# Kernel tuning notes

Measured on AMD Instinct MI355X. Metric: run time of the kernel, lower is better.

Reference implementation:

```python
import jax, jax.numpy as jnp
import numpy as np

N = 50000
E = 1600000
EP = 500000
D_IN, D_EMB = 64, 32


def setup_inputs() -> dict:
    key = jax.random.key(0)
    ks = jax.random.split(key, 12)
    return {
        "x": jax.random.normal(ks[0], (N, D_IN), dtype=jnp.float32),
        "W1": jax.random.normal(ks[1], (D_IN, D_EMB), dtype=jnp.float32) * (1.0 / np.sqrt(D_IN)),
        "b1": jnp.zeros((D_EMB,), dtype=jnp.float32),
        "W2": jax.random.normal(ks[2], (D_EMB, 2 * D_EMB), dtype=jnp.float32) * (1.0 / np.sqrt(D_EMB)),
        "b2": jnp.zeros((2 * D_EMB,), dtype=jnp.float32),
        "eps": jax.random.normal(ks[3], (N, D_EMB), dtype=jnp.float32),
        "edge_src": jax.random.randint(ks[4], (E,), 0, N, dtype=jnp.int32),
        "edge_dst": jax.random.randint(ks[5], (E,), 0, N, dtype=jnp.int32),
        "pos_src": jax.random.randint(ks[6], (EP,), 0, N, dtype=jnp.int32),
        "pos_dst": jax.random.randint(ks[7], (EP,), 0, N, dtype=jnp.int32),
        "neg_src": jax.random.randint(ks[8], (EP,), 0, N, dtype=jnp.int32),
        "neg_dst": jax.random.randint(ks[9], (EP,), 0, N, dtype=jnp.int32),
    }


def _degree_norms(src, dst, n):
    ones = jnp.ones(src.shape, dtype=jnp.float32)
    out_deg = jax.ops.segment_sum(ones, src, num_segments=n)
    in_deg = jax.ops.segment_sum(ones, dst, num_segments=n)
    # DGL GraphConv norm='both': clamp degrees to >=1, pow(-0.5)
    return jnp.clip(out_deg, 1.0) ** -0.5, jnp.clip(in_deg, 1.0) ** -0.5


def _graph_conv(h, src, dst, norm_src, norm_dst, W, b, n):
    # rst = D_dst^{-1/2} A D_src^{-1/2} h W + b
    msg = (h * norm_src[:, None])[src]                       # [E, d] gather
    agg = jax.ops.segment_sum(msg, dst, num_segments=n)      # [N, d] scatter-add
    return (agg * norm_dst[:, None]) @ W + b


def _dot_predict(z, u, v):
    # u_dot_v: per-edge inner product of endpoint embeddings
    return jnp.sum(z[u] * z[v], axis=-1)


def reference(x, W1, b1, W2, b2, eps, edge_src, edge_dst,
              pos_src, pos_dst, neg_src, neg_dst):
    n = x.shape[0]
    ns, nd = _degree_norms(edge_src, edge_dst, n)
    h = _graph_conv(x, edge_src, edge_dst, ns, nd, W1, b1, n)
    h = jax.nn.relu(h)  # dropout = identity (eval mode)
    h = _graph_conv(h, edge_src, edge_dst, ns, nd, W2, b2, n)
    mu, log_var = jnp.split(h, 2, axis=-1)
    sigma = jnp.exp(log_var / 2.0)
    z = mu + sigma * eps
    pos = _dot_predict(z, pos_src, pos_dst)
    neg = _dot_predict(z, neg_src, neg_dst)
    return pos, neg, mu, sigma
```

## Files before the change

### kernel.cpp

```cpp
#include <hip/hip_runtime.h>
#include <math.h>

#define NN  50000
#define NE  1600000
#define NEP 500000
#define DIN 64
#define DE  32

#define BKT_SH 7
#define NB     391
#define S1B    250
#define CHK    6400
#define HB     128
#define HCHK   12500
#define HWRD   12500
#define XWB    3125

__device__ __forceinline__ unsigned f2b(float f) {
    unsigned u = __float_as_uint(f);
    return (u + 0x7FFFu + ((u >> 16) & 1u)) >> 16;
}
__device__ __forceinline__ unsigned pack2(float a, float b) {
    return f2b(a) | (f2b(b) << 16);
}
__device__ __forceinline__ float blo(unsigned u) { return __uint_as_float(u << 16); }
__device__ __forceinline__ float bhi(unsigned u) { return __uint_as_float(u & 0xFFFF0000u); }

__global__ __launch_bounds__(256) void k_h1s1(const int* __restrict__ src,
                                              const int* __restrict__ dst,
                                              unsigned* __restrict__ partial,
                                              int* __restrict__ T) {
    __shared__ unsigned h[HWRD];
    int t = threadIdx.x;
    if (blockIdx.x < HB) {
        for (int i = t; i < HWRD; i += 256) h[i] = 0;
        __syncthreads();
        int beg = blockIdx.x * HCHK;
        for (int i = beg + t; i < beg + HCHK; i += 256) {
            int s = src[i];
            atomicAdd(&h[s >> 2], 1u << ((s & 3) * 8));
        }
        __syncthreads();
        unsigned* p = partial + (size_t)blockIdx.x * HWRD;
        for (int i = t; i < HWRD; i += 256) p[i] = h[i];
    } else {
        int b = blockIdx.x - HB;
        int* cd = (int*)h;
        for (int i = t; i < NB; i += 256) cd[i] = 0;
        __syncthreads();
        int beg = b * CHK;
        for (int i = beg + t; i < beg + CHK; i += 256)
            atomicAdd(&cd[dst[i] >> BKT_SH], 1);
        __syncthreads();
        for (int i = t; i < NB; i += 256) T[b * NB + i] = cd[i];
    }
}

__global__ __launch_bounds__(512) void k_s2h(const int* __restrict__ T,
                                             int* __restrict__ Base,
                                             int* __restrict__ BS,
                                             const unsigned* __restrict__ partial,
                                             int* __restrict__ degs) {
    int t = threadIdx.x;
    if (blockIdx.x == 0) {
        __shared__ int tot[512];
        int run = 0;
        if (t < NB) {
            for (int b = 0; b < S1B; b++) {
                Base[b * NB + t] = run;
                run += T[b * NB + t];
            }
        }
        tot[t] = (t < NB) ? run : 0;
        __syncthreads();
        for (int off = 1; off < 512; off <<= 1) {
            int v = (t >= off) ? tot[t - off] : 0;
            __syncthreads();
            tot[t] += v;
            __syncthreads();
        }
        if (t < NB) BS[t] = (t == 0) ? 0 : tot[t - 1];
        if (t == 0) BS[NB] = NE;
    } else {
        int w = (blockIdx.x - 1) * 512 + t;
        if (w < HWRD) {
            int c0 = 0, c1 = 0, c2 = 0, c3 = 0;
            for (int b = 0; b < HB; b++) {
                unsigned v = partial[(size_t)b * HWRD + w];
                c0 += (int)(v & 0xFFu);
                c1 += (int)((v >> 8) & 0xFFu);
                c2 += (int)((v >> 16) & 0xFFu);
                c3 += (int)(v >> 24);
            }
            ((int4*)degs)[w] = make_int4(c0, c1, c2, c3);
        }
    }
}

__global__ __launch_bounds__(512) void k_s3(const int* __restrict__ src,
                                            const int* __restrict__ dst,
                                            const int* __restrict__ T,
                                            const int* __restrict__ Base,
                                            const int* __restrict__ BS,
                                            unsigned* __restrict__ tmp) {
    __shared__ int scn[512];
    __shared__ int delta[NB];
    __shared__ int cur[NB];
    __shared__ unsigned buf[CHK];
    int t = threadIdx.x;
    int beg = blockIdx.x * CHK;
    scn[t] = (t < NB) ? T[blockIdx.x * NB + t] : 0;
    __syncthreads();
    for (int off = 1; off < 512; off <<= 1) {
        int v = (t >= off) ? scn[t - off] : 0;
        __syncthreads();
        scn[t] += v;
        __syncthreads();
    }
    if (t < NB) {
        int ls = (t == 0) ? 0 : scn[t - 1];
        cur[t] = ls;
        delta[t] = Base[blockIdx.x * NB + t] + BS[t] - ls;
    }
    __syncthreads();
    for (int i = t; i < CHK; i += 512) {
        int d = dst[beg + i];
        int s = src[beg + i];
        int lp = atomicAdd(&cur[d >> BKT_SH], 1);
        buf[lp] = (unsigned)s | ((unsigned)d << 16);
    }
    __syncthreads();
    for (int i = t; i < CHK; i += 512) {
        unsigned e = buf[i];
        tmp[delta[e >> (16 + BKT_SH)] + i] = e;
    }
}

__global__ __launch_bounds__(256) void k_s4x(const unsigned* __restrict__ tmp,
                                             const int* __restrict__ BS,
                                             int* __restrict__ csr,
                                             int* __restrict__ rowptr,
                                             const float* __restrict__ x,
                                             const float* __restrict__ W1,
                                             const int* __restrict__ degs,
                                             unsigned* __restrict__ xw1b) {
    __shared__ int sh[8576];
    int t = threadIdx.x;
    if (blockIdx.x < NB) {
        int* cnt = sh;
        int* scn = sh + 128;
        int* cur = sh + 256;
        int* srcbuf = sh + 384;
        int p = blockIdx.x;
        int ebeg = BS[p], eend = BS[p + 1];
        int ne = eend - ebeg;
        if (t < 128) cnt[t] = 0;
        __syncthreads();
        for (int i = t; i < ne; i += 256)
            atomicAdd(&cnt[(tmp[ebeg + i] >> 16) & 127], 1);
        __syncthreads();
        if (t < 128) scn[t] = cnt[t];
        __syncthreads();
        for (int off = 1; off < 128; off <<= 1) {
            int v = 0;
            if (t < 128 && t >= off) v = scn[t - off];
            __syncthreads();
            if (t < 128) scn[t] += v;
            __syncthreads();
        }
        if (t < 128) {
            int ex = (t == 0) ? 0 : scn[t - 1];
            cur[t] = ex;
            int node = (p << BKT_SH) + t;
            if (node < NN) rowptr[node] = ebeg + ex;
        }
        if (p == NB - 1 && t == 0) rowptr[NN] = NE;
        __syncthreads();
        for (int i = t; i < ne; i += 256) {
            unsigned e = tmp[ebeg + i];
            int lp = atomicAdd(&cur[(e >> 16) & 127], 1);
            srcbuf[lp] = (int)(e & 0xFFFFu);
        }
        __syncthreads();
        for (int i = t; i < ne; i += 256)
            csr[ebeg + i] = srcbuf[i];
    } else {
        float* sW = (float*)sh;
        for (int i = t; i < DIN * DE; i += 256) sW[i] = W1[i];
        __syncthreads();
        int r  = (blockIdx.x - NB) * 16 + (t >> 4);
        int tc = t & 15;
        const float* xr = x + (size_t)r * DIN;
        float a0 = 0.f, a1 = 0.f;
#pragma unroll
        for (int k = 0; k < DIN; k++) {
            float v = xr[k];
            a0 += v * sW[k * DE + 2 * tc];
            a1 += v * sW[k * DE + 2 * tc + 1];
        }
        float ns = rsqrtf(fmaxf((float)degs[r], 1.0f));
        xw1b[r * 16 + tc] = pack2(a0 * ns, a1 * ns);
    }
}

__device__ __forceinline__ void acc8(float* a, uint4 w) {
    a[0] += blo(w.x); a[1] += bhi(w.x);
    a[2] += blo(w.y); a[3] += bhi(w.y);
    a[4] += blo(w.z); a[5] += bhi(w.z);
    a[6] += blo(w.w); a[7] += bhi(w.w);
}

__device__ __forceinline__ void gather_row(const int* __restrict__ csr,
                                           const uint4* __restrict__ msg,
                                           int beg, int end, int l, float* a) {
    int idx = beg;
    for (; idx + 8 <= end; idx += 8) {
        int s0 = csr[idx],     s1 = csr[idx + 1], s2 = csr[idx + 2], s3 = csr[idx + 3];
        int s4 = csr[idx + 4], s5 = csr[idx + 5], s6 = csr[idx + 6], s7 = csr[idx + 7];
        uint4 w0 = msg[s0 * 4 + l];
        uint4 w1 = msg[s1 * 4 + l];
        uint4 w2 = msg[s2 * 4 + l];
        uint4 w3 = msg[s3 * 4 + l];
        uint4 w4 = msg[s4 * 4 + l];
        uint4 w5 = msg[s5 * 4 + l];
        uint4 w6 = msg[s6 * 4 + l];
        uint4 w7 = msg[s7 * 4 + l];
        acc8(a, w0); acc8(a, w1); acc8(a, w2); acc8(a, w3);
        acc8(a, w4); acc8(a, w5); acc8(a, w6); acc8(a, w7);
    }
    for (; idx + 4 <= end; idx += 4) {
        int s0 = csr[idx], s1 = csr[idx + 1], s2 = csr[idx + 2], s3 = csr[idx + 3];
        uint4 w0 = msg[s0 * 4 + l];
        uint4 w1 = msg[s1 * 4 + l];
        uint4 w2 = msg[s2 * 4 + l];
        uint4 w3 = msg[s3 * 4 + l];
        acc8(a, w0); acc8(a, w1); acc8(a, w2); acc8(a, w3);
    }
    for (; idx < end; idx++) {
        uint4 w = msg[csr[idx] * 4 + l];
        acc8(a, w);
    }
}

__global__ __launch_bounds__(256) void k_g1(const int* __restrict__ rowptr,
                                            const int* __restrict__ csr,
                                            const uint4* __restrict__ msg,
                                            const int* __restrict__ degs,
                                            const float* __restrict__ b1,
                                            uint4* __restrict__ out) {
    int t = blockIdx.x * 256 + threadIdx.x;
    int r = t >> 2;
    int l = t & 3;
    if (r >= NN) return;
    int beg = rowptr[r];
    int end = rowptr[r + 1];
    float a[8] = {0, 0, 0, 0, 0, 0, 0, 0};
    gather_row(csr, msg, beg, end, l, a);
    float scd = rsqrtf(fmaxf((float)(end - beg), 1.0f));
    float scs = rsqrtf(fmaxf((float)degs[r], 1.0f));
    const float4* b14 = (const float4*)b1;
    float4 bb0 = b14[2 * l], bb1 = b14[2 * l + 1];
    float o0 = fmaxf(scd * a[0] + bb0.x, 0.f) * scs;
    float o1 = fmaxf(scd * a[1] + bb0.y, 0.f) * scs;
    float o2 = fmaxf(scd * a[2] + bb0.z, 0.f) * scs;
    float o3 = fmaxf(scd * a[3] + bb0.w, 0.f) * scs;
    float o4 = fmaxf(scd * a[4] + bb1.x, 0.f) * scs;
    float o5 = fmaxf(scd * a[5] + bb1.y, 0.f) * scs;
    float o6 = fmaxf(scd * a[6] + bb1.z, 0.f) * scs;
    float o7 = fmaxf(scd * a[7] + bb1.w, 0.f) * scs;
    out[r * 4 + l] = make_uint4(pack2(o0, o1), pack2(o2, o3), pack2(o4, o5), pack2(o6, o7));
}

__global__ __launch_bounds__(256) void k_g2f(const int* __restrict__ rowptr,
                                             const int* __restrict__ csr,
                                             const uint4* __restrict__ msg,
                                             const float* __restrict__ W2,
                                             const float* __restrict__ b2,
                                             const float* __restrict__ eps,
                                             float* __restrict__ mu,
                                             float* __restrict__ sigma,
                                             unsigned* __restrict__ zb) {
    __shared__ float sW[DE * 64];
    __shared__ float sb[64];
    int t = threadIdx.x;
    for (int i = t; i < DE * 64; i += 256) sW[i] = W2[i];
    if (t < 64) sb[t] = b2[t];
    __syncthreads();
    int g = blockIdx.x * 256 + t;
    int r = g >> 2;
    int l = g & 3;
    if (r >= NN) return;
    int beg = rowptr[r];
    int end = rowptr[r + 1];
    float a[8] = {0, 0, 0, 0, 0, 0, 0, 0};
    gather_row(csr, msg, beg, end, l, a);
    float scd = rsqrtf(fmaxf((float)(end - beg), 1.0f));
#pragma unroll
    for (int k = 0; k < 8; k++) a[k] *= scd;
    float o[64];
#pragma unroll
    for (int c = 0; c < 64; c++) o[c] = 0.f;
    const float* wbase = sW + 8 * l * 64;
#pragma unroll
    for (int k = 0; k < 8; k++) {
        float av = a[k];
        const float* wrow = wbase + k * 64;
#pragma unroll
        for (int c = 0; c < 64; c++) o[c] += av * wrow[c];
    }
    float o2[32];
#pragma unroll
    for (int j = 0; j < 32; j++) {
        float send = (l < 2) ? o[32 + j] : o[j];
        float recv = __shfl_xor(send, 2);
        o2[j] = ((l < 2) ? o[j] : o[32 + j]) + recv;
    }
    float o3[16];
#pragma unroll
    for (int j = 0; j < 16; j++) {
        float send = ((l & 1) == 0) ? o2[16 + j] : o2[j];
        float recv = __shfl_xor(send, 1);
        o3[j] = (((l & 1) == 0) ? o2[j] : o2[16 + j]) + recv;
    }
    int cbase = 16 * l;
#pragma unroll
    for (int j = 0; j < 16; j++) o3[j] += sb[cbase + j];
    if (l < 2) {
        float4* mp = (float4*)(mu + (size_t)r * DE + 16 * l);
        mp[0] = make_float4(o3[0],  o3[1],  o3[2],  o3[3]);
        mp[1] = make_float4(o3[4],  o3[5],  o3[6],  o3[7]);
        mp[2] = make_float4(o3[8],  o3[9],  o3[10], o3[11]);
        mp[3] = make_float4(o3[12], o3[13], o3[14], o3[15]);
    }
    float muv[16];
#pragma unroll
    for (int j = 0; j < 16; j++) muv[j] = __shfl_xor(o3[j], 2);
    if (l >= 2) {
        int cc = 16 * (l - 2);
        const float4* ep = (const float4*)(eps + (size_t)r * DE + cc);
        float4 e0 = ep[0], e1 = ep[1], e2 = ep[2], e3 = ep[3];
        float ev[16] = {e0.x, e0.y, e0.z, e0.w, e1.x, e1.y, e1.z, e1.w,
                        e2.x, e2.y, e2.z, e2.w, e3.x, e3.y, e3.z, e3.w};
        float sgv[16], zv[16];
#pragma unroll
        for (int j = 0; j < 16; j++) {
            sgv[j] = expf(0.5f * o3[j]);
            zv[j]  = muv[j] + sgv[j] * ev[j];
        }
        float4* sp = (float4*)(sigma + (size_t)r * DE + cc);
        sp[0] = make_float4(sgv[0],  sgv[1],  sgv[2],  sgv[3]);
        sp[1] = make_float4(sgv[4],  sgv[5],  sgv[6],  sgv[7]);
        sp[2] = make_float4(sgv[8],  sgv[9],  sgv[10], sgv[11]);
        sp[3] = make_float4(sgv[12], sgv[13], sgv[14], sgv[15]);
        uint4* zp = (uint4*)(zb + (size_t)r * 16 + (l - 2) * 8);
        zp[0] = make_uint4(pack2(zv[0], zv[1]), pack2(zv[2], zv[3]),
                           pack2(zv[4], zv[5]), pack2(zv[6], zv[7]));
        zp[1] = make_uint4(pack2(zv[8],  zv[9]),  pack2(zv[10], zv[11]),
                           pack2(zv[12], zv[13]), pack2(zv[14], zv[15]));
    }
}

__global__ __launch_bounds__(256) void k_dot2(const uint4* __restrict__ zb4,
                                              const int* __restrict__ pu,
                                              const int* __restrict__ pv,
                                              const int* __restrict__ nu,
                                              const int* __restrict__ nv,
                                              float* __restrict__ out) {
    int t = blockIdx.x * 256 + threadIdx.x;
    int e = t >> 2;
    int l = t & 3;
    if (e < 2 * NEP) {
        int ee = (e < NEP) ? e : e - NEP;
        const int* uu = (e < NEP) ? pu : nu;
        const int* vv = (e < NEP) ? pv : nv;
        int a = uu[ee];
        int b = vv[ee];
        uint4 za = zb4[a * 4 + l];
        uint4 zc = zb4[b * 4 + l];
        float s = blo(za.x) * blo(zc.x) + bhi(za.x) * bhi(zc.x)
                + blo(za.y) * blo(zc.y) + bhi(za.y) * bhi(zc.y)
                + blo(za.z) * blo(zc.z) + bhi(za.z) * bhi(zc.z)
                + blo(za.w) * blo(zc.w) + bhi(za.w) * bhi(zc.w);
        s += __shfl_xor(s, 1);
        s += __shfl_xor(s, 2);
        if (l == 0) out[e] = s;
    }
}

extern "C" void kernel_launch(void* const* d_in, const int* in_sizes, int n_in,
                              void* d_out, int out_size, void* d_ws, size_t ws_size,
                              hipStream_t stream) {
    const float* x    = (const float*)d_in[0];
    const float* W1   = (const float*)d_in[1];
    const float* b1   = (const float*)d_in[2];
    const float* W2   = (const float*)d_in[3];
    const float* b2   = (const float*)d_in[4];
    const float* eps  = (const float*)d_in[5];
    const int*   esrc = (const int*)d_in[6];
    const int*   edst = (const int*)d_in[7];
    const int*   psrc = (const int*)d_in[8];
    const int*   pdst = (const int*)d_in[9];
    const int*   gsrc = (const int*)d_in[10];
    const int*   gdst = (const int*)d_in[11];

    float* out = (float*)d_out;
    float* pos = out;
    float* mu  = out + 2 * NEP;
    float* sg  = out + 2 * NEP + NN * DE;

    int* wi = (int*)d_ws;
    int*      rowptr  = wi;
    int*      T       = wi + 50001;
    int*      Base    = wi + 147751;
    int*      BS      = wi + 245501;
    int*      degs    = wi + 245896;
    int*      csr     = wi + 295896;
    unsigned* partial = (unsigned*)(wi + 1895896);
    unsigned* tmp     = (unsigned*)(wi + 3495896);
    unsigned* P0      = (unsigned*)(wi + 5095896);
    unsigned* P1      = P0 + 16 * NN;

    k_h1s1<<<HB + S1B, 256, 0, stream>>>(esrc, edst, partial, T);
    k_s2h <<<1 + (HWRD + 511) / 512, 512, 0, stream>>>(T, Base, BS, partial, degs);
    k_s3  <<<S1B, 512, 0, stream>>>(esrc, edst, T, Base, BS, tmp);
    k_s4x <<<NB + XWB, 256, 0, stream>>>(tmp, BS, csr, rowptr, x, W1, degs, P0);
    k_g1  <<<(NN * 4 + 255) / 256, 256, 0, stream>>>(rowptr, csr, (const uint4*)P0, degs, b1, (uint4*)P1);
    k_g2f <<<(NN * 4 + 255) / 256, 256, 0, stream>>>(rowptr, csr, (const uint4*)P1, W2, b2, eps, mu, sg, P0);
    k_dot2<<<(2 * NEP * 4) / 256, 256, 0, stream>>>((const uint4*)P0, psrc, pdst, gsrc, gdst, pos);
}
```

Baseline: 231.7 us.

## Shuffle aggregated inputs instead of partial outputs in layer-2 transform; drop CSR staging buffer

In the layer-2 kernel, each lane used to compute a full 64-wide partial output and reduce it across the 4 lanes with shuffles. Now the lanes exchange their 8 aggregated input values, and each lane computes only its own 16 output columns over all 32 inputs. This removes the 64-float accumulator and should cut register pressure, at the cost of more shuffles of inputs. Separately, the CSR build writes source ids straight to global memory at their atomically assigned slot, skipping the shared staging buffer and one barrier, which shrinks LDS use but makes the global writes scattered.

After: 216.7 us. 1.07x faster.

```diff
diff --git a/kernel.cpp b/kernel.cpp
--- a/kernel.cpp
+++ b/kernel.cpp
@@ -144,13 +144,12 @@
                                              const float* __restrict__ W1,
                                              const int* __restrict__ degs,
                                              unsigned* __restrict__ xw1b) {
-    __shared__ int sh[8576];
+    __shared__ float sW[DIN * DE];
     int t = threadIdx.x;
     if (blockIdx.x < NB) {
-        int* cnt = sh;
-        int* scn = sh + 128;
-        int* cur = sh + 256;
-        int* srcbuf = sh + 384;
+        int* cnt = (int*)sW;
+        int* scn = cnt + 128;
+        int* cur = cnt + 256;
         int p = blockIdx.x;
         int ebeg = BS[p], eend = BS[p + 1];
         int ne = eend - ebeg;
@@ -179,13 +178,9 @@
         for (int i = t; i < ne; i += 256) {
             unsigned e = tmp[ebeg + i];
             int lp = atomicAdd(&cur[(e >> 16) & 127], 1);
-            srcbuf[lp] = (int)(e & 0xFFFFu);
-        }
-        __syncthreads();
-        for (int i = t; i < ne; i += 256)
-            csr[ebeg + i] = srcbuf[i];
+            csr[ebeg + lp] = (int)(e & 0xFFFFu);
+        }
     } else {
-        float* sW = (float*)sh;
         for (int i = t; i < DIN * DE; i += 256) sW[i] = W1[i];
         __syncthreads();
         int r  = (blockIdx.x - NB) * 16 + (t >> 4);
@@ -297,34 +292,21 @@
     float scd = rsqrtf(fmaxf((float)(end - beg), 1.0f));
 #pragma unroll
     for (int k = 0; k < 8; k++) a[k] *= scd;
-    float o[64];
-#pragma unroll
-    for (int c = 0; c < 64; c++) o[c] = 0.f;
-    const float* wbase = sW + 8 * l * 64;
-#pragma unroll
-    for (int k = 0; k < 8; k++) {
-        float av = a[k];
-        const float* wrow = wbase + k * 64;
-#pragma unroll
-        for (int c = 0; c < 64; c++) o[c] += av * wrow[c];
-    }
-    float o2[32];
-#pragma unroll
-    for (int j = 0; j < 32; j++) {
-        float send = (l < 2) ? o[32 + j] : o[j];
-        float recv = __shfl_xor(send, 2);
-        o2[j] = ((l < 2) ? o[j] : o[32 + j]) + recv;
-    }
+    int cbase = 16 * l;
     float o3[16];
 #pragma unroll
-    for (int j = 0; j < 16; j++) {
-        float send = ((l & 1) == 0) ? o2[16 + j] : o2[j];
-        float recv = __shfl_xor(send, 1);
-        o3[j] = (((l & 1) == 0) ? o2[j] : o2[16 + j]) + recv;
-    }
-    int cbase = 16 * l;
-#pragma unroll
-    for (int j = 0; j < 16; j++) o3[j] += sb[cbase + j];
+    for (int j = 0; j < 16; j++) o3[j] = sb[cbase + j];
+#pragma unroll
+    for (int d = 0; d < 4; d++) {
+        int kb = 8 * (l ^ d);
+#pragma unroll
+        for (int k = 0; k < 8; k++) {
+            float av = (d == 0) ? a[k] : __shfl_xor(a[k], d);
+            const float* wrow = sW + (kb + k) * 64 + cbase;
+#pragma unroll
+            for (int j = 0; j < 16; j++) o3[j] += av * wrow[j];
+        }
+    }
     if (l < 2) {
         float4* mp = (float4*)(mu + (size_t)r * DE + 16 * l);
         mp[0] = make_float4(o3[0],  o3[1],  o3[2],  o3[3]);
```
